# Kernel optimization log

Measured on AMD Instinct MI355X. Metric: run time of the kernel, lower is better.

The kernel has to match this reference:

```python
import jax, jax.numpy as jnp
import numpy as np
from jax import lax

B, T, E, D = 16, 4096, 512, 128
LOCAL_SIZE, SUMMARY_FREQ = 64, 32
LN_EPS = 1e-5


def setup_inputs() -> dict:
    key = jax.random.key(0)
    ks = jax.random.split(key, 12)
    p = lambda k, s: 0.1 * jax.random.normal(k, s, jnp.float32) + 0.01
    return {
        "x": jax.random.normal(ks[0], (B, T, E), jnp.float32),
        "local_state_control": p(ks[1], (D, D)),
        "local_input_influence": p(ks[2], (E, D)),
        "local_blend_shaper": p(ks[3], (D, D)),
        "global_summary_state_control": p(ks[4], (D, D)),
        "global_summary_state_influence": p(ks[5], (E, D)),
        "global_summary_output_shaper": p(ks[6], (D, D)),
        "global_state_control": p(ks[7], (D, D)),
        "global_input_influence": p(ks[8], (E, D)),
        "global_output_shaper": p(ks[9], (D, E)),
        "ln_gamma": jnp.ones((D,), jnp.float32),
        "ln_beta": jnp.zeros((D,), jnp.float32),
        "lin_w": 0.02 * jax.random.normal(ks[10], (E, E), jnp.float32),
        "lin_b": jnp.zeros((E,), jnp.float32),
        "local_size": LOCAL_SIZE,
        "summary_frequency": SUMMARY_FREQ,
    }


def _ln(h, g, b):
    m = jnp.mean(h, -1, keepdims=True)
    v = jnp.var(h, -1, keepdims=True)
    return (h - m) * lax.rsqrt(v + LN_EPS) * g + b


def reference(x, local_state_control, local_input_influence, local_blend_shaper,
              global_summary_state_control, global_summary_state_influence,
              global_summary_output_shaper, global_state_control,
              global_input_influence, global_output_shaper,
              ln_gamma, ln_beta, lin_w, lin_b, local_size, summary_frequency):
    # Dropout layers are identity in inference mode.
    Bb, Tt, Ee = x.shape
    Dd = ln_gamma.shape[0]
    t_idx = jnp.arange(Tt)

    # ---- Local windowed recurrence, vectorized across all timesteps t. ----
    # Original: for each t, local_state starts at 0 and consumes tokens
    # t-1, t-2, ..., max(0, t-local_size) in that (reverse) order.
    # We scan over window offset j; at step j, timestep t consumes token t-1-j.
    x_pad = jnp.pad(x, ((0, 0), (local_size, 0), (0, 0)))  # pad front of time axis

    def local_step(S, j):  # S: [B, T, D]
        # X[:, t, :] == x[:, t-1-j, :] (zeros where out of range)
        X = lax.dynamic_slice_in_dim(x_pad, local_size - 1 - j, Tt, axis=1)
        valid = (t_idx >= j + 1)[None, :, None]  # token index t-1-j >= 0
        S_new = _ln(S @ local_state_control + X @ local_input_influence, ln_gamma, ln_beta)
        return jnp.where(valid, S_new, S), None

    S0 = jnp.zeros((Bb, Tt, Dd), x.dtype)
    S_local, _ = lax.scan(local_step, S0, jnp.arange(local_size))
    blended = S_local @ local_blend_shaper  # [B, T, D]

    # ---- Global sequential recurrence over time. ----
    is_summary = (t_idx % summary_frequency) == (summary_frequency - 1)

    def gstep(carry, inp):
        g, summ = carry  # [B, D], [B, D]
        x_t, loc_t, flag = inp
        g = _ln(g @ global_state_control + x_t @ global_input_influence + loc_t + summ,
                ln_gamma, ln_beta)
        out_t = g @ global_output_shaper  # [B, E]
        summ_new = _ln(summ @ global_summary_state_control +
                       out_t @ global_summary_state_influence,
                       ln_gamma, ln_beta) @ global_summary_output_shaper
        summ = jnp.where(flag, summ_new, summ)
        return (g, summ), out_t

    init = (jnp.zeros((Bb, Dd), x.dtype), jnp.zeros((Bb, Dd), x.dtype))
    _, outs = lax.scan(gstep, init,
                       (x.transpose(1, 0, 2), blended.transpose(1, 0, 2), is_summary))
    out = outs.transpose(1, 0, 2)  # [B, T, E]
    return out @ lin_w.T + lin_b
```

## Files before the change

### kernel.cpp

```cpp
#include <hip/hip_runtime.h>
#include <stdint.h>


typedef unsigned short u16;
typedef unsigned int   u32;
typedef __attribute__((ext_vector_type(8))) short bf16x8;
typedef __attribute__((ext_vector_type(4))) float f32x4;
typedef __attribute__((ext_vector_type(2))) u32   u32x2;
typedef __attribute__((ext_vector_type(4))) u32   u32x4;

#define MFMA16(a,b,c) __builtin_amdgcn_mfma_f32_16x16x32_bf16((a),(b),(c),0,0,0)

static constexpr int T_SEQ   = 4096;
static constexpr int CHUNK_C = 64;
static constexpr int WARM_C  = 256;
static constexpr int PF      = 4;

__device__ __forceinline__ u32 bf16rne(float x){
  u32 u = __float_as_uint(x);
  return (u + 0x7FFFu + ((u >> 16) & 1u)) >> 16;
}
__device__ __forceinline__ u32 rne_hi(u32 u){
  return u + 0x7FFFu + ((u >> 16) & 1u);
}
__device__ __forceinline__ u32 pk2(float lo, float hi){
  return __builtin_amdgcn_perm(rne_hi(__float_as_uint(hi)),
                               rne_hi(__float_as_uint(lo)), 0x07060302u);
}
__device__ __forceinline__ float bflo(u32 p){ return __uint_as_float(p << 16); }
__device__ __forceinline__ float bfhi(u32 p){ return __uint_as_float(p & 0xFFFF0000u); }

__device__ __forceinline__ bf16x8 mk8(u32x2 a, u32x2 b){
  union { u32 u[4]; bf16x8 v; } t;
  t.u[0] = a.x; t.u[1] = a.y; t.u[2] = b.x; t.u[3] = b.y;
  return t.v;
}

__device__ __forceinline__ int kperm(int s){
  return (s & 0xE0) | ((s & 4) << 2) | ((s >> 1) & 0x0C) | (s & 3);
}

__device__ __forceinline__ float xsum4(float v){
#if __has_builtin(__builtin_amdgcn_permlane16_swap) && __has_builtin(__builtin_amdgcn_permlane32_swap)
  typedef __attribute__((ext_vector_type(2))) unsigned pl2u;
  pl2u a = __builtin_amdgcn_permlane16_swap(__float_as_uint(v), __float_as_uint(v),
                                            false, false);
  float s = __uint_as_float(a.x) + __uint_as_float(a.y);
  pl2u b = __builtin_amdgcn_permlane32_swap(__float_as_uint(s), __float_as_uint(s),
                                            false, false);
  return __uint_as_float(b.x) + __uint_as_float(b.y);
#else
  v += __shfl_xor(v, 16, 64);
  v += __shfl_xor(v, 32, 64);
  return v;
#endif
}

__device__ __forceinline__ void ln_stats(const f32x4 (&C)[8], float &rs, float &mr){
  float s4[8], q4[8];
#pragma unroll
  for (int mt = 0; mt < 8; ++mt){
    float a = C[mt][0] + C[mt][1], b = C[mt][2] + C[mt][3];
    s4[mt] = a + b;
    float p = C[mt][0]*C[mt][0]; p = __builtin_fmaf(C[mt][1], C[mt][1], p);
    float r = C[mt][2]*C[mt][2]; r = __builtin_fmaf(C[mt][3], C[mt][3], r);
    q4[mt] = p + r;
  }
  float s  = ((s4[0]+s4[1])+(s4[2]+s4[3])) + ((s4[4]+s4[5])+(s4[6]+s4[7]));
  float ss = ((q4[0]+q4[1])+(q4[2]+q4[3])) + ((q4[4]+q4[5])+(q4[6]+q4[7]));
  s  = xsum4(s);
  ss = xsum4(ss);
  float mean = s * 0.0078125f;
  float var  = __builtin_fmaf(ss, 0.0078125f, -mean*mean);
  rs = rsqrtf(var + 1e-5f);
  mr = mean * rs;
}

__global__ void prep_fold(const float* lsc, const float* lbs, const float* gsc,
                          const float* gssc, const float* gsos,
                          const float* lii, const float* gii, const float* gamma,
                          u16* WlscA, u16* WlbsA, u16* WgcA,
                          u16* WsscA, u16* WssoA, u16* WcatA){
  int id = blockIdx.x * 256 + threadIdx.x;
  if (id < 81920){
    int m = id >> 14;
    int r = id & 16383;
    int j = r >> 7, k = r & 127;
    int kd = kperm(k);
    float g = gamma[kd];
    float v = 0.f; u16* dst = WlscA;
    switch (m){
      case 0: v = g * lsc[kd*128 + j];  dst = WlscA; break;
      case 1: v = g * lbs[kd*128 + j];  dst = WlbsA; break;
      case 2: v = g * gsc[kd*128 + j];  dst = WgcA;  break;
      case 3: v =     gssc[kd*128 + j]; dst = WsscA; break;
      default: v = g * gsos[kd*128 + j]; dst = WssoA; break;
    }
    dst[j*128 + k] = (u16)bf16rne(v);
  } else {
    int r = id - 81920;
    int m = r >> 9, k = r & 511;
    float v = (m < 128) ? lii[k*128 + m] : gii[k*128 + (m - 128)];
    WcatA[m*512 + k] = (u16)bf16rne(v);
  }
}

__global__ void prep_dot(const float* gos, const float* gssi, const float* linw,
                         const float* gamma, const float* beta,
                         u16* Wsi2A, u16* WfinA, float* bout){
  int id = blockIdx.x * 256 + threadIdx.x;
  if (id < 16384){
    int j = id >> 7, k = id & 127;
    int kd = kperm(k);
    float s = 0.f;
    for (int e = 0; e < 512; ++e) s += gos[kd*512 + e] * gssi[e*128 + j];
    Wsi2A[j*128 + k] = (u16)bf16rne(gamma[kd] * s);
  } else if (id < 81920){
    int r = id - 16384;
    int f = r >> 7, k = r & 127;
    float s = 0.f;
    for (int e = 0; e < 512; ++e) s += gos[k*512 + e] * linw[f*512 + e];
    WfinA[f*128 + k] = (u16)bf16rne(gamma[k] * s);
  } else {
    int e = id - 81920;
    float s = 0.f;
    for (int d = 0; d < 128; ++d) s += beta[d] * gos[d*512 + e];
    bout[e] = s;
  }
}

__global__ void prep_vec(const float* lsc, const float* lbs, const float* gsc,
                         const float* gsos, const float* gssi,
                         const float* linw, const float* linb,
                         const float* gamma, const float* beta, const float* bout,
                         float* biaslsc, float* badd, float* bsi, float* bso,
                         float* bfin, u16* y0){
  int t = threadIdx.x;
  if (t < 128){
    float s1 = 0.f, s2 = 0.f, s3 = 0.f;
    for (int k = 0; k < 128; ++k){
      float bk = beta[k];
      s1 += bk * lsc[k*128 + t];
      s2 += bk * (lbs[k*128 + t] + gsc[k*128 + t]);
      s3 += bk * gsos[k*128 + t];
    }
    biaslsc[t] = s1; badd[t] = s2; bso[t] = s3;
    float s4 = 0.f;
    for (int e = 0; e < 512; ++e) s4 += bout[e] * gssi[e*128 + t];
    bsi[t] = s4;
    y0[t] = (u16)bf16rne(-beta[t] / gamma[t]);
  }
  float s5 = 0.f;
  for (int e = 0; e < 512; ++e) s5 += bout[e] * linw[t*512 + e];
  bfin[t] = s5 + linb[t];
}

__global__ __launch_bounds__(256, 2)
void stageA(const float* x, const u16* WcatA, const float* biaslsc,
            u16* U, float* R){
  __shared__ u16 Wl[256 * 40];
  __shared__ u16 Xl[64 * 40];
  const int t0 = blockIdx.x * 64;
  const int tid = threadIdx.x;
  const int w = tid >> 6, lane = tid & 63, ln = lane & 15, q = lane >> 4;

  f32x4 C[4][4];
#pragma unroll
  for (int a = 0; a < 4; ++a)
#pragma unroll
    for (int b = 0; b < 4; ++b) C[a][b] = (f32x4)0.f;

  const int ti = tid >> 2, p = tid & 3;
  for (int kc = 0; kc < 16; ++kc){
    {
      const u16* src = WcatA + tid*512 + kc*32;
#pragma unroll
      for (int i = 0; i < 4; ++i)
        *(u32x4*)&Wl[tid*40 + i*8] = *(const u32x4*)(src + i*8);
      const float* xs = x + (size_t)(t0 + ti)*512 + kc*32 + p*8;
      f32x4 xa = *(const f32x4*)(xs);
      f32x4 xb = *(const f32x4*)(xs + 4);
      u32x4 xw = { pk2(xa[0],xa[1]), pk2(xa[2],xa[3]),
                   pk2(xb[0],xb[1]), pk2(xb[2],xb[3]) };
      *(u32x4*)&Xl[ti*40 + p*8] = xw;
    }
    __syncthreads();
    bf16x8 Af[4], Bf[4];
#pragma unroll
    for (int mt = 0; mt < 4; ++mt)
      Af[mt] = *(const bf16x8*)&Wl[(16*(4*w + mt) + ln)*40 + 8*q];
#pragma unroll
    for (int nt = 0; nt < 4; ++nt)
      Bf[nt] = *(const bf16x8*)&Xl[(16*nt + ln)*40 + 8*q];
#pragma unroll
    for (int mt = 0; mt < 4; ++mt)
#pragma unroll
      for (int nt = 0; nt < 4; ++nt)
        C[mt][nt] = MFMA16(Af[mt], Bf[nt], C[mt][nt]);
    __syncthreads();
  }
#pragma unroll
  for (int mt = 0; mt < 4; ++mt){
    int mg = 64*w + 16*mt + 4*q;
    if (mg < 128){
      f32x4 bl = *(const f32x4*)(biaslsc + mg);
#pragma unroll
      for (int nt = 0; nt < 4; ++nt){
        int row = t0 + 16*nt + ln;
        u32x2 pv = { pk2(C[mt][nt][0] + bl[0], C[mt][nt][1] + bl[1]),
                     pk2(C[mt][nt][2] + bl[2], C[mt][nt][3] + bl[3]) };
        *(u32x2*)(U + (size_t)row*128 + mg) = pv;
      }
    } else {
      int d = mg - 128;
#pragma unroll
      for (int nt = 0; nt < 4; ++nt){
        int row = t0 + 16*nt + ln;
        *(f32x4*)(R + (size_t)row*128 + d) = C[mt][nt];
      }
    }
  }
}

__global__ __launch_bounds__(256, 2)
void stageB(const u16* U, const u16* WlscA, const u16* WlbsA,
            const float* badd, const u16* y0, float* R){
  __shared__ u16 Ul[128 * 136];
  const int b = blockIdx.x >> 6, ch = blockIdx.x & 63;
  const int t0 = ch * 64;
  const int tid = threadIdx.x;
  const int w = tid >> 6, lane = tid & 63, ln = lane & 15, q = lane >> 4;
  const int rowb = b * T_SEQ;

  for (int u = tid; u < 2048; u += 256){
    int r = u >> 4, c = u & 15;
    int rg = t0 - 64 + r; if (rg < 0) rg = 0;
    u32x4 v = *(const u32x4*)(U + (size_t)(rowb + rg)*128 + c*8);
    *(u32x4*)&Ul[r*136 + c*8] = v;
  }
  u32x2 yp[8];
#pragma unroll
  for (int mt = 0; mt < 8; ++mt)
    yp[mt] = *(const u32x2*)(y0 + 16*mt + 4*q);
  __syncthreads();

  bf16x8 A[8][4];
#pragma unroll
  for (int mt = 0; mt < 8; ++mt)
#pragma unroll
    for (int kt = 0; kt < 4; ++kt)
      A[mt][kt] = *(const bf16x8*)(WlscA + (16*mt + ln)*128 + 32*kt + 8*q);

  const int tl = t0 + 16*w + ln;
  for (int j = 0; j < 64; ++j){
    const int lr = 64 + 16*w + ln - 1 - j;
    f32x4 C[8];
#pragma unroll
    for (int mt = 0; mt < 8; ++mt){
      u32x2 uv = *(const u32x2*)&Ul[lr*136 + 16*mt + 4*q];
      C[mt][0] = bflo(uv.x); C[mt][1] = bfhi(uv.x);
      C[mt][2] = bflo(uv.y); C[mt][3] = bfhi(uv.y);
    }
    bf16x8 Bf[4];
#pragma unroll
    for (int kt = 0; kt < 4; ++kt)
      Bf[kt] = mk8(yp[2*kt], yp[2*kt+1]);
#pragma unroll
    for (int mt = 0; mt < 8; ++mt)
#pragma unroll
      for (int kt = 0; kt < 4; ++kt)
        C[mt] = MFMA16(A[mt][kt], Bf[kt], C[mt]);
    float rs, mr; ln_stats(C, rs, mr);
    if (tl >= j + 1){
#pragma unroll
      for (int mt = 0; mt < 8; ++mt){
        yp[mt].x = pk2(__builtin_fmaf(C[mt][0], rs, -mr),
                       __builtin_fmaf(C[mt][1], rs, -mr));
        yp[mt].y = pk2(__builtin_fmaf(C[mt][2], rs, -mr),
                       __builtin_fmaf(C[mt][3], rs, -mr));
      }
    }
  }

#pragma unroll
  for (int mt = 0; mt < 8; ++mt)
#pragma unroll
    for (int kt = 0; kt < 4; ++kt)
      A[mt][kt] = *(const bf16x8*)(WlbsA + (16*mt + ln)*128 + 32*kt + 8*q);
  bf16x8 Bf[4];
#pragma unroll
  for (int kt = 0; kt < 4; ++kt)
    Bf[kt] = mk8(yp[2*kt], yp[2*kt+1]);
  f32x4 C[8];
#pragma unroll
  for (int mt = 0; mt < 8; ++mt)
    C[mt] = *(const f32x4*)(badd + 16*mt + 4*q);
#pragma unroll
  for (int mt = 0; mt < 8; ++mt)
#pragma unroll
    for (int kt = 0; kt < 4; ++kt)
      C[mt] = MFMA16(A[mt][kt], Bf[kt], C[mt]);
#pragma unroll
  for (int mt = 0; mt < 8; ++mt){
    float* rp = R + (size_t)(rowb + tl)*128 + 16*mt + 4*q;
    f32x4 rv = *(const f32x4*)rp;
    *(f32x4*)rp = C[mt] + rv;
  }
}

__global__ __launch_bounds__(64, 1)
void stageC(const float* R, const u16* WgcA, const u16* WsscA,
            const u16* Wsi2A, const u16* WssoA,
            const float* bsi, const float* bso, const u16* y0, u16* Y){
  const int c0 = blockIdx.x * CHUNK_C;
  const int ts = (c0 - WARM_C > 0) ? (c0 - WARM_C) : 0;
  const int te = c0 + CHUNK_C;
  const int lane = threadIdx.x, ln = lane & 15, q = lane >> 4;
  const int rb = ln * T_SEQ;

  u32x2 yp[8];
#pragma unroll
  for (int mt = 0; mt < 8; ++mt)
    yp[mt] = *(const u32x2*)(y0 + 16*mt + 4*q);

  bf16x8 A[8][4];
#pragma unroll
  for (int mt = 0; mt < 8; ++mt)
#pragma unroll
    for (int kt = 0; kt < 4; ++kt)
      A[mt][kt] = *(const bf16x8*)(WgcA + (16*mt + ln)*128 + 32*kt + 8*q);

  f32x4 summ[8];
#pragma unroll
  for (int mt = 0; mt < 8; ++mt) summ[mt] = (f32x4)0.f;

  f32x4 Rb[PF][8];
#pragma unroll
  for (int p = 0; p < PF; ++p)
#pragma unroll
    for (int mt = 0; mt < 8; ++mt)
      Rb[p][mt] = *(const f32x4*)(R + (size_t)(rb + ts + p)*128 + 16*mt + 4*q);

  for (int t = ts; t < te; t += PF){
#pragma unroll
    for (int p = 0; p < PF; ++p){
      const int tt = t + p;

      f32x4 C[8];
#pragma unroll
      for (int mt = 0; mt < 8; ++mt) C[mt] = Rb[p][mt] + summ[mt];

      int tn = tt + PF; if (tn > te - 1) tn = te - 1;
#pragma unroll
      for (int mt = 0; mt < 8; ++mt)
        Rb[p][mt] = *(const f32x4*)(R + (size_t)(rb + tn)*128 + 16*mt + 4*q);

      bf16x8 Bf[4];
#pragma unroll
      for (int kt = 0; kt < 4; ++kt)
        Bf[kt] = mk8(yp[2*kt], yp[2*kt+1]);
#pragma unroll
      for (int mt = 0; mt < 8; ++mt)
#pragma unroll
        for (int kt = 0; kt < 4; ++kt)
          C[mt] = MFMA16(A[mt][kt], Bf[kt], C[mt]);
      float rs, mr; ln_stats(C, rs, mr);
#pragma unroll
      for (int mt = 0; mt < 8; ++mt){
        yp[mt].x = pk2(__builtin_fmaf(C[mt][0], rs, -mr),
                       __builtin_fmaf(C[mt][1], rs, -mr));
        yp[mt].y = pk2(__builtin_fmaf(C[mt][2], rs, -mr),
                       __builtin_fmaf(C[mt][3], rs, -mr));
      }
      if (tt >= c0){
#pragma unroll
        for (int mt = 0; mt < 8; ++mt)
          *(u32x2*)(Y + (size_t)(rb + tt)*128 + 16*mt + 4*q) = yp[mt];
      }
      if ((tt & 31) == 31){
        bf16x8 Sf[4], Yf[4];
        u32x2 sp[8];
#pragma unroll
        for (int mt = 0; mt < 8; ++mt){
          sp[mt].x = pk2(summ[mt][0], summ[mt][1]);
          sp[mt].y = pk2(summ[mt][2], summ[mt][3]);
        }
#pragma unroll
        for (int kt = 0; kt < 4; ++kt){
          Sf[kt] = mk8(sp[2*kt], sp[2*kt+1]);
          Yf[kt] = mk8(yp[2*kt], yp[2*kt+1]);
        }
        f32x4 Cz[8];
#pragma unroll
        for (int mt = 0; mt < 8; ++mt)
          Cz[mt] = *(const f32x4*)(bsi + 16*mt + 4*q);
#pragma unroll
        for (int mt = 0; mt < 8; ++mt)
#pragma unroll
          for (int kt = 0; kt < 4; ++kt){
            bf16x8 Aw = *(const bf16x8*)(WsscA + (16*mt + ln)*128 + 32*kt + 8*q);
            Cz[mt] = MFMA16(Aw, Sf[kt], Cz[mt]);
          }
#pragma unroll
        for (int mt = 0; mt < 8; ++mt)
#pragma unroll
          for (int kt = 0; kt < 4; ++kt){
            bf16x8 Aw = *(const bf16x8*)(Wsi2A + (16*mt + ln)*128 + 32*kt + 8*q);
            Cz[mt] = MFMA16(Aw, Yf[kt], Cz[mt]);
          }
        float rz, mz; ln_stats(Cz, rz, mz);
        u32x2 zp[8];
#pragma unroll
        for (int mt = 0; mt < 8; ++mt){
          zp[mt].x = pk2(__builtin_fmaf(Cz[mt][0], rz, -mz),
                         __builtin_fmaf(Cz[mt][1], rz, -mz));
          zp[mt].y = pk2(__builtin_fmaf(Cz[mt][2], rz, -mz),
                         __builtin_fmaf(Cz[mt][3], rz, -mz));
        }
        bf16x8 Zf[4];
#pragma unroll
        for (int kt = 0; kt < 4; ++kt)
          Zf[kt] = mk8(zp[2*kt], zp[2*kt+1]);
        f32x4 Cs[8];
#pragma unroll
        for (int mt = 0; mt < 8; ++mt)
          Cs[mt] = *(const f32x4*)(bso + 16*mt + 4*q);
#pragma unroll
        for (int mt = 0; mt < 8; ++mt)
#pragma unroll
          for (int kt = 0; kt < 4; ++kt){
            bf16x8 Aw = *(const bf16x8*)(WssoA + (16*mt + ln)*128 + 32*kt + 8*q);
            Cs[mt] = MFMA16(Aw, Zf[kt], Cs[mt]);
          }
#pragma unroll
        for (int mt = 0; mt < 8; ++mt) summ[mt] = Cs[mt];
      }
    }
  }
}

__global__ __launch_bounds__(256, 2)
void stageD(const u16* Y, const u16* WfinA, const float* bfin, float* Out){
  __shared__ u16 Yl[32 * 136];
  const size_t row0 = (size_t)blockIdx.x * 32;
  const int tid = threadIdx.x;
  const int w = tid >> 6, lane = tid & 63, ln = lane & 15, q = lane >> 4;

  for (int u = tid; u < 512; u += 256){
    int r = u >> 4, c = u & 15;
    u32x4 v = *(const u32x4*)(Y + (row0 + r)*128 + c*8);
    *(u32x4*)&Yl[r*136 + c*8] = v;
  }
  __syncthreads();

  bf16x8 A[8][4];
#pragma unroll
  for (int mt = 0; mt < 8; ++mt)
#pragma unroll
    for (int kt = 0; kt < 4; ++kt)
      A[mt][kt] = *(const bf16x8*)(WfinA + (size_t)(128*w + 16*mt + ln)*128 + 32*kt + 8*q);
  bf16x8 Bf[2][4];
#pragma unroll
  for (int nt = 0; nt < 2; ++nt)
#pragma unroll
    for (int kt = 0; kt < 4; ++kt)
      Bf[nt][kt] = *(const bf16x8*)&Yl[(16*nt + ln)*136 + 32*kt + 8*q];
  f32x4 C[8][2];
#pragma unroll
  for (int mt = 0; mt < 8; ++mt)
#pragma unroll
    for (int nt = 0; nt < 2; ++nt) C[mt][nt] = (f32x4)0.f;
#pragma unroll
  for (int mt = 0; mt < 8; ++mt)
#pragma unroll
    for (int nt = 0; nt < 2; ++nt)
#pragma unroll
      for (int kt = 0; kt < 4; ++kt)
        C[mt][nt] = MFMA16(A[mt][kt], Bf[nt][kt], C[mt][nt]);
#pragma unroll
  for (int mt = 0; mt < 8; ++mt){
    f32x4 bv = *(const f32x4*)(bfin + 128*w + 16*mt + 4*q);
#pragma unroll
    for (int nt = 0; nt < 2; ++nt){
      f32x4 o = C[mt][nt] + bv;
      *(f32x4*)(Out + (row0 + 16*nt + ln)*512 + 128*w + 16*mt + 4*q) = o;
    }
  }
}

extern "C" void kernel_launch(void* const* d_in, const int* in_sizes, int n_in,
                              void* d_out, int out_size, void* d_ws, size_t ws_size,
                              hipStream_t stream) {
  const float* x    = (const float*)d_in[0];
  const float* lsc  = (const float*)d_in[1];
  const float* lii  = (const float*)d_in[2];
  const float* lbs  = (const float*)d_in[3];
  const float* gssc = (const float*)d_in[4];
  const float* gssi = (const float*)d_in[5];
  const float* gsos = (const float*)d_in[6];
  const float* gsc  = (const float*)d_in[7];
  const float* gii  = (const float*)d_in[8];
  const float* gos  = (const float*)d_in[9];
  const float* gam  = (const float*)d_in[10];
  const float* bet  = (const float*)d_in[11];
  const float* linw = (const float*)d_in[12];
  const float* linb = (const float*)d_in[13];
  (void)in_sizes; (void)n_in; (void)out_size; (void)ws_size;

  char* w8 = (char*)d_ws;
  float* R       = (float*)(w8);
  u16*   U       = (u16*)  (w8 + 33554432);
  u16*   Y       = (u16*)  (w8 + 50331648);
  u16*   WcatA   = (u16*)  (w8 + 67108864);
  u16*   WlscA   = (u16*)  (w8 + 67371008);
  u16*   WlbsA   = (u16*)  (w8 + 67403776);
  u16*   WgcA    = (u16*)  (w8 + 67436544);
  u16*   WsscA   = (u16*)  (w8 + 67469312);
  u16*   WssoA   = (u16*)  (w8 + 67502080);
  u16*   Wsi2A   = (u16*)  (w8 + 67534848);
  u16*   WfinA   = (u16*)  (w8 + 67567616);
  float* biaslsc = (float*)(w8 + 67698688);
  float* badd    = (float*)(w8 + 67699200);
  float* bsi     = (float*)(w8 + 67699712);
  float* bso     = (float*)(w8 + 67700224);
  float* bout    = (float*)(w8 + 67700736);
  float* bfin    = (float*)(w8 + 67702784);
  u16*   y0      = (u16*)  (w8 + 67704832);

  prep_fold<<<832, 256, 0, stream>>>(lsc, lbs, gsc, gssc, gsos, lii, gii, gam,
                                     WlscA, WlbsA, WgcA, WsscA, WssoA, WcatA);
  prep_dot <<<322, 256, 0, stream>>>(gos, gssi, linw, gam, bet, Wsi2A, WfinA, bout);
  prep_vec <<<1, 512, 0, stream>>>(lsc, lbs, gsc, gsos, gssi, linw, linb,
                                   gam, bet, bout, biaslsc, badd, bsi, bso, bfin, y0);
  stageA<<<1024, 256, 0, stream>>>(x, WcatA, biaslsc, U, R);
  stageB<<<1024, 256, 0, stream>>>(U, WlscA, WlbsA, badd, y0, R);
  stageC<<<64, 64, 0, stream>>>(R, WgcA, WsscA, Wsi2A, WssoA, bsi, bso, y0, Y);
  stageD<<<2048, 256, 0, stream>>>(Y, WfinA, bfin, (float*)d_out);
}
```

Measured before the change: 967.7 us.

## Stream stageC recurrence inputs through LDS ring with manual waitcnt pipelining

The serial global recurrence kernel now prefetches each step's R rows straight into an LDS ring buffer with global_load_lds and reads them back with ds_read_b128. Prefetch, wait and store are ordered by hand with explicit vmcnt/lgkmcnt waits and sched barriers. Output stores become unconditional inline-asm stores, redirected to a dump buffer (the reused U scratch) during warm-up steps, so the branch disappears. The y state is kept as a 4-deep rotating register set so the waits can cover stores still in flight, and bf16 packing switches to the hardware v_cvt_pk_bf16_f32 instruction. The aim is to cut latency on the single-wave critical path, at the cost of fragile hand-tuned counters and more register pressure.

```diff
diff --git a/kernel.cpp b/kernel.cpp
--- a/kernel.cpp
+++ b/kernel.cpp
@@ -14,7 +14,6 @@
 static constexpr int T_SEQ   = 4096;
 static constexpr int CHUNK_C = 64;
 static constexpr int WARM_C  = 256;
-static constexpr int PF      = 4;
 
 __device__ __forceinline__ u32 bf16rne(float x){
   u32 u = __float_as_uint(x);
@@ -26,6 +25,11 @@
 __device__ __forceinline__ u32 pk2(float lo, float hi){
   return __builtin_amdgcn_perm(rne_hi(__float_as_uint(hi)),
                                rne_hi(__float_as_uint(lo)), 0x07060302u);
+}
+__device__ __forceinline__ u32 cvtpk(float lo, float hi){
+  u32 r;
+  asm("v_cvt_pk_bf16_f32 %0, %1, %2" : "=v"(r) : "v"(lo), "v"(hi));
+  return r;
 }
 __device__ __forceinline__ float bflo(u32 p){ return __uint_as_float(p << 16); }
 __device__ __forceinline__ float bfhi(u32 p){ return __uint_as_float(p & 0xFFFF0000u); }
@@ -34,6 +38,12 @@
   union { u32 u[4]; bf16x8 v; } t;
   t.u[0] = a.x; t.u[1] = a.y; t.u[2] = b.x; t.u[3] = b.y;
   return t.v;
+}
+
+__device__ __forceinline__ void gload_lds16(const float* g, void* l){
+  __builtin_amdgcn_global_load_lds(
+      (const __attribute__((address_space(1))) void*)g,
+      (__attribute__((address_space(3))) void*)l, 16, 0, 0);
 }
 
 __device__ __forceinline__ int kperm(int s){
@@ -311,17 +321,15 @@
 __global__ __launch_bounds__(64, 1)
 void stageC(const float* R, const u16* WgcA, const u16* WsscA,
             const u16* Wsi2A, const u16* WssoA,
-            const float* bsi, const float* bso, const u16* y0, u16* Y){
+            const float* bsi, const float* bso, const u16* y0, u16* Y,
+            u16* dump){
+  __shared__ f32x4 ring[2048];
   const int c0 = blockIdx.x * CHUNK_C;
   const int ts = (c0 - WARM_C > 0) ? (c0 - WARM_C) : 0;
   const int te = c0 + CHUNK_C;
   const int lane = threadIdx.x, ln = lane & 15, q = lane >> 4;
   const int rb = ln * T_SEQ;
-
-  u32x2 yp[8];
-#pragma unroll
-  for (int mt = 0; mt < 8; ++mt)
-    yp[mt] = *(const u32x2*)(y0 + 16*mt + 4*q);
+  const u32 lbase = (u32)lane * 16u;
 
   bf16x8 A[8][4];
 #pragma unroll
@@ -330,35 +338,76 @@
     for (int kt = 0; kt < 4; ++kt)
       A[mt][kt] = *(const bf16x8*)(WgcA + (16*mt + ln)*128 + 32*kt + 8*q);
 
+  u32x2 ypb[4][8];
+#pragma unroll
+  for (int mt = 0; mt < 8; ++mt){
+    u32x2 v = *(const u32x2*)(y0 + 16*mt + 4*q);
+    ypb[0][mt] = v; ypb[1][mt] = v; ypb[2][mt] = v; ypb[3][mt] = v;
+  }
+
+#pragma unroll
+  for (int mt = 0; mt < 8; ++mt){
+    asm volatile("" :: "v"(A[mt][0]), "v"(A[mt][1]), "v"(A[mt][2]), "v"(A[mt][3]));
+    asm volatile("" :: "v"(ypb[0][mt]), "v"(ypb[1][mt]),
+                       "v"(ypb[2][mt]), "v"(ypb[3][mt]));
+  }
+
   f32x4 summ[8];
 #pragma unroll
   for (int mt = 0; mt < 8; ++mt) summ[mt] = (f32x4)0.f;
 
-  f32x4 Rb[PF][8];
-#pragma unroll
-  for (int p = 0; p < PF; ++p)
+  u16* const dumpl = dump + (size_t)blockIdx.x * 8192 + (size_t)lane * 128;
+
+#pragma unroll
+  for (int p = 0; p < 4; ++p){
+    const float* ra = R + (size_t)(rb + ts + p)*128 + 4*q;
 #pragma unroll
     for (int mt = 0; mt < 8; ++mt)
-      Rb[p][mt] = *(const f32x4*)(R + (size_t)(rb + ts + p)*128 + 16*mt + 4*q);
-
-  for (int t = ts; t < te; t += PF){
-#pragma unroll
-    for (int p = 0; p < PF; ++p){
-      const int tt = t + p;
+      gload_lds16(ra + 16*mt, (char*)ring + p*8192 + mt*1024);
+  }
+  asm volatile("s_waitcnt vmcnt(0)" ::: "memory");
+  __builtin_amdgcn_sched_barrier(0);
+
+  const int ngroups = (te - ts) >> 2;
+  for (int g = 0; g < ngroups; ++g){
+    const int tb = ts + g*4;
+#pragma unroll
+    for (int p = 0; p < 4; ++p){
+      const int tt = tb + p;
+
+      asm volatile("s_waitcnt vmcnt(48)"
+        :: "v"(ypb[p][0]), "v"(ypb[p][1]), "v"(ypb[p][2]), "v"(ypb[p][3]),
+           "v"(ypb[p][4]), "v"(ypb[p][5]), "v"(ypb[p][6]), "v"(ypb[p][7])
+        : "memory");
+      __builtin_amdgcn_sched_barrier(0);
+
+      u32x4 D[8];
+#pragma unroll
+      for (int mt = 0; mt < 8; ++mt)
+        asm volatile("ds_read_b128 %0, %1 offset:%c2"
+                     : "=v"(D[mt]) : "v"(lbase), "i"(p*8192 + mt*1024));
+      asm volatile("s_waitcnt lgkmcnt(0)" ::: "memory");
+      __builtin_amdgcn_sched_barrier(0);
+
+      {
+        int tn = tt + 4; if (tn > te - 1) tn = te - 1;
+        const float* ra = R + (size_t)(rb + tn)*128 + 4*q;
+#pragma unroll
+        for (int mt = 0; mt < 8; ++mt)
+          gload_lds16(ra + 16*mt, (char*)ring + p*8192 + mt*1024);
+      }
 
       f32x4 C[8];
 #pragma unroll
-      for (int mt = 0; mt < 8; ++mt) C[mt] = Rb[p][mt] + summ[mt];
-
-      int tn = tt + PF; if (tn > te - 1) tn = te - 1;
-#pragma unroll
-      for (int mt = 0; mt < 8; ++mt)
-        Rb[p][mt] = *(const f32x4*)(R + (size_t)(rb + tn)*128 + 16*mt + 4*q);
+      for (int mt = 0; mt < 8; ++mt){
+        union { u32x4 u; f32x4 f; } cv; cv.u = D[mt];
+        C[mt] = cv.f + summ[mt];
+      }
 
       bf16x8 Bf[4];
 #pragma unroll
       for (int kt = 0; kt < 4; ++kt)
-        Bf[kt] = mk8(yp[2*kt], yp[2*kt+1]);
+        Bf[kt] = mk8(ypb[(p+3)&3][2*kt], ypb[(p+3)&3][2*kt+1]);
 #pragma unroll
       for (int mt = 0; mt < 8; ++mt)
 #pragma unroll
@@ -367,28 +416,32 @@
       float rs, mr; ln_stats(C, rs, mr);
 #pragma unroll
       for (int mt = 0; mt < 8; ++mt){
-        yp[mt].x = pk2(__builtin_fmaf(C[mt][0], rs, -mr),
-                       __builtin_fmaf(C[mt][1], rs, -mr));
-        yp[mt].y = pk2(__builtin_fmaf(C[mt][2], rs, -mr),
-                       __builtin_fmaf(C[mt][3], rs, -mr));
-      }
-      if (tt >= c0){
-#pragma unroll
-        for (int mt = 0; mt < 8; ++mt)
-          *(u32x2*)(Y + (size_t)(rb + tt)*128 + 16*mt + 4*q) = yp[mt];
-      }
-      if ((tt & 31) == 31){
+        ypb[p][mt].x = cvtpk(__builtin_fmaf(C[mt][0], rs, -mr),
+                             __builtin_fmaf(C[mt][1], rs, -mr));
+        ypb[p][mt].y = cvtpk(__builtin_fmaf(C[mt][2], rs, -mr),
+                             __builtin_fmaf(C[mt][3], rs, -mr));
+      }
+
+      u16* yt = (tt >= c0)
+        ? (u16*)((char*)Y + (((size_t)(rb + tt)) << 8) + 8*q)
+        : dumpl;
+#pragma unroll
+      for (int mt = 0; mt < 8; ++mt)
+        asm volatile("global_store_dwordx2 %0, %1, off offset:%c2"
+                     :: "v"(yt), "v"(ypb[p][mt]), "i"(mt*32) : "memory");
+
+      if (p == 3 && ((tt & 31) == 31)){
         bf16x8 Sf[4], Yf[4];
         u32x2 sp[8];
 #pragma unroll
         for (int mt = 0; mt < 8; ++mt){
-          sp[mt].x = pk2(summ[mt][0], summ[mt][1]);
-          sp[mt].y = pk2(summ[mt][2], summ[mt][3]);
+          sp[mt].x = cvtpk(summ[mt][0], summ[mt][1]);
+          sp[mt].y = cvtpk(summ[mt][2], summ[mt][3]);
         }
 #pragma unroll
         for (int kt = 0; kt < 4; ++kt){
           Sf[kt] = mk8(sp[2*kt], sp[2*kt+1]);
-          Yf[kt] = mk8(yp[2*kt], yp[2*kt+1]);
+          Yf[kt] = mk8(ypb[3][2*kt], ypb[3][2*kt+1]);
         }
         f32x4 Cz[8];
 #pragma unroll
@@ -412,10 +465,10 @@
         u32x2 zp[8];
 #pragma unroll
         for (int mt = 0; mt < 8; ++mt){
-          zp[mt].x = pk2(__builtin_fmaf(Cz[mt][0], rz, -mz),
-                         __builtin_fmaf(Cz[mt][1], rz, -mz));
-          zp[mt].y = pk2(__builtin_fmaf(Cz[mt][2], rz, -mz),
-                         __builtin_fmaf(Cz[mt][3], rz, -mz));
+          zp[mt].x = cvtpk(__builtin_fmaf(Cz[mt][0], rz, -mz),
+                           __builtin_fmaf(Cz[mt][1], rz, -mz));
+          zp[mt].y = cvtpk(__builtin_fmaf(Cz[mt][2], rz, -mz),
+                           __builtin_fmaf(Cz[mt][3], rz, -mz));
         }
         bf16x8 Zf[4];
 #pragma unroll
@@ -437,6 +490,7 @@
       }
     }
   }
+  asm volatile("s_waitcnt vmcnt(0)" ::: "memory");
 }
 
 __global__ __launch_bounds__(256, 2)
@@ -534,6 +588,6 @@
                                    gam, bet, bout, biaslsc, badd, bsi, bso, bfin, y0);
   stageA<<<1024, 256, 0, stream>>>(x, WcatA, biaslsc, U, R);
   stageB<<<1024, 256, 0, stream>>>(U, WlscA, WlbsA, badd, y0, R);
-  stageC<<<64, 64, 0, stream>>>(R, WgcA, WsscA, Wsi2A, WssoA, bsi, bso, y0, Y);
+  stageC<<<64, 64, 0, stream>>>(R, WgcA, WsscA, Wsi2A, WssoA, bsi, bso, y0, Y, U);
   stageD<<<2048, 256, 0, stream>>>(Y, WfinA, bfin, (float*)d_out);
 }
```

Result: no change. 983.0 us (+1.6%).
